# Performance work log

Measured on AMD Instinct MI355X. Metric: run time of the kernel, lower is better.

Reference implementation:

```python
import jax, jax.numpy as jnp
import numpy as np

N = 100000
E = 1600000
F = 64
THETA = (0.6, -0.4, 0.3, -0.2, 0.1)  # k = 5 polynomial coefficients


def setup_inputs() -> dict:
    key = jax.random.key(0)
    kx, ke = jax.random.split(key)
    x = jax.random.normal(kx, (N, F), dtype=jnp.float32)
    edge_index = jax.random.randint(ke, (2, E), 0, N, dtype=jnp.int64)
    return {"x": x, "edge_index": edge_index}


def _l_sym_mul(feat, src, dst, deg_inv_sqrt, n):
    # L_sym * feat = feat - D^{-1/2} A D^{-1/2} feat
    src_norm = feat[src] * deg_inv_sqrt[src]            # [E, F] gather + scale
    agg = jax.ops.segment_sum(src_norm, dst, num_segments=n)  # scatter-add to dst
    return feat - deg_inv_sqrt * agg


def reference(x, edge_index):
    src, dst = edge_index[0], edge_index[1]
    n = x.shape[0]
    # in-degree from dst, clamp to >= 1, D^{-1/2} as [N, 1]
    deg = jax.ops.segment_sum(jnp.ones((src.shape[0],), dtype=x.dtype), dst,
                              num_segments=n)
    deg = jnp.maximum(deg, 1.0)[:, None]
    deg_inv_sqrt = deg ** -0.5

    h_acc = THETA[0] * x
    feat = x
    for k in range(1, len(THETA)):
        feat = _l_sym_mul(feat, src, dst, deg_inv_sqrt, n)
        h_acc = h_acc + THETA[k] * feat
    return h_acc
```

## Files before the change

kernel.cpp:

```cpp
#include <hip/hip_runtime.h>
#include <hip/hip_fp16.h>


constexpr int kF = 64;
constexpr int BSHIFT = 8;
constexpr int NB = 1 << BSHIFT;
constexpr int TILE = 2048;
constexpr int KMAX = 512;

typedef unsigned nv4u __attribute__((ext_vector_type(4)));
typedef float    nv4f __attribute__((ext_vector_type(4)));

static __device__ __forceinline__ float hlo(unsigned u) {
    return __half2float(__ushort_as_half((unsigned short)(u & 0xffffu)));
}
static __device__ __forceinline__ float hhi(unsigned u) {
    return __half2float(__ushort_as_half((unsigned short)(u >> 16)));
}
static __device__ __forceinline__ unsigned pack2h(float a, float b) {
    return (unsigned)__half_as_ushort(__float2half_rn(a)) |
           ((unsigned)__half_as_ushort(__float2half_rn(b)) << 16);
}
static __device__ __forceinline__ unsigned padd2(unsigned a, unsigned b) {
    __half2 ha = *reinterpret_cast<__half2*>(&a);
    __half2 hb = *reinterpret_cast<__half2*>(&b);
    __half2 hc = __hadd2(ha, hb);
    return *reinterpret_cast<unsigned*>(&hc);
}

__global__ void k_binA(const int* __restrict__ src, const int* __restrict__ dst,
                       unsigned* __restrict__ pairs, int* __restrict__ gcursor,
                       const float4* __restrict__ x4, uint4* __restrict__ xb4,
                       int n8, int E, int K, int cap) {
    __shared__ int hist[KMAX];
    __shared__ int gb[KMAX];
    const int tid = threadIdx.x;
    const long long tb = (long long)blockIdx.x * TILE;
    const int tcount = (int)min((long long)TILE, (long long)E - tb);

    {
        int per = (n8 + gridDim.x - 1) / (int)gridDim.x;
        int b0 = blockIdx.x * per;
        int b1 = min(b0 + per, n8);
        for (int i = b0 + tid; i < b1; i += 512) {
            float4 a = x4[2 * i];
            float4 b = x4[2 * i + 1];
            uint4 o;
            o.x = pack2h(a.x, a.y);
            o.y = pack2h(a.z, a.w);
            o.z = pack2h(b.x, b.y);
            o.w = pack2h(b.z, b.w);
            xb4[i] = o;
        }
    }

    hist[tid] = 0;
    __syncthreads();
    int dc[4], sc[4];
    #pragma unroll
    for (int k = 0; k < 4; ++k) {
        int i = tid + k * 512;
        if (i < tcount) {
            dc[k] = dst[tb + i];
            sc[k] = src[tb + i];
            atomicAdd(&hist[dc[k] >> BSHIFT], 1);
        } else {
            dc[k] = -1;
        }
    }
    __syncthreads();
    int hv = hist[tid];
    gb[tid] = (tid < K && hv > 0) ? atomicAdd(&gcursor[tid], hv) : 0;
    hist[tid] = 0;
    __syncthreads();
    #pragma unroll
    for (int k = 0; k < 4; ++k) {
        if (dc[k] >= 0) {
            int d = dc[k];
            int b = d >> BSHIFT;
            int pos = atomicAdd(&hist[b], 1);
            pairs[(size_t)b * cap + gb[b] + pos] =
                ((unsigned)(d & (NB - 1)) << 23) | (unsigned)sc[k];
        }
    }
}

__global__ void k_binB(const unsigned* __restrict__ pairs, const int* __restrict__ gcursor,
                       int* __restrict__ rp, float* __restrict__ dinv2,
                       float* __restrict__ rdeg, int* __restrict__ csr,
                       const uint4* __restrict__ xb, uint4* __restrict__ g0,
                       int N, int E, int K, int cap) {
    __shared__ int gsc[KMAX];
    __shared__ int cnt[NB];
    __shared__ int stmp[NB];
    __shared__ int cur[NB];
    __shared__ float sdinv[NB];
    const int b = blockIdx.x;
    const int tid = threadIdx.x;

    if (b == 0 && tid < 8)
        g0[((size_t)N << 3) + tid] = make_uint4(0, 0, 0, 0);

    int gv = (tid < K) ? gcursor[tid] : 0;
    gsc[tid] = gv;
    __syncthreads();
    for (int o = 1; o < KMAX; o <<= 1) {
        int t = (tid >= o) ? gsc[tid - o] : 0;
        __syncthreads();
        gsc[tid] += t;
        __syncthreads();
    }
    const int ecnt = gcursor[b];
    const int base = gsc[b] - ecnt;
    const unsigned* bp = pairs + (size_t)b * cap;

    if (tid < NB) cnt[tid] = 0;
    __syncthreads();
    for (int i = tid; i < ecnt; i += 512)
        atomicAdd(&cnt[bp[i] >> 23], 1);
    __syncthreads();
    int v = (tid < NB) ? cnt[tid] : 0;
    if (tid < NB) stmp[tid] = v;
    __syncthreads();
    for (int o = 1; o < NB; o <<= 1) {
        int t = (tid >= o && tid < NB) ? stmp[tid - o] : 0;
        __syncthreads();
        if (tid < NB) stmp[tid] += t;
        __syncthreads();
    }
    int node = (b << BSHIFT) + tid;
    if (tid < NB) {
        int abs0 = base + stmp[tid] - v;
        cur[tid] = abs0;
        float d = fmaxf((float)v, 1.0f);
        sdinv[tid] = rsqrtf(d);
        if (node < N) {
            rp[node] = abs0;
            dinv2[node] = 1.0f / d;
            rdeg[node]  = sqrtf(d);
        }
    }
    if (b == K - 1 && tid == 0) rp[N] = E;
    __syncthreads();
    for (int i = tid; i < ecnt; i += 512) {
        unsigned p = bp[i];
        int pos = atomicAdd(&cur[p >> 23], 1);
        csr[pos] = (int)(p & 0x7FFFFFu);
    }
    const int nbase = b << BSHIFT;
    const int qmax = min(NB, N - nbase) << 3;
    const uint4* xbp = xb + ((size_t)nbase << 3);
    uint4* g0p = g0 + ((size_t)nbase << 3);
    for (int q = tid; q < qmax; q += 512) {
        float di = sdinv[q >> 3];
        uint4 xv = xbp[q];
        uint4 o;
        o.x = pack2h(di * hlo(xv.x), di * hhi(xv.x));
        o.y = pack2h(di * hlo(xv.y), di * hhi(xv.y));
        o.z = pack2h(di * hlo(xv.z), di * hhi(xv.z));
        o.w = pack2h(di * hlo(xv.w), di * hhi(xv.w));
        g0p[q] = o;
    }
}

template <bool LAST>
__global__ void k_gather(const int* __restrict__ rp, const int* __restrict__ csr,
                         const unsigned short* __restrict__ gin,
                         const float* __restrict__ dinv2,
                         unsigned short* __restrict__ gout,
                         const unsigned short* __restrict__ xb,
                         const unsigned short* __restrict__ g1t,
                         const unsigned short* __restrict__ g2t,
                         const float* __restrict__ rdeg,
                         float* __restrict__ h, int n,
                         float t0, float t1, float t2, float t3, float t4) {
    if (!LAST && blockIdx.x == 0 && threadIdx.x < 8)
        *(((uint4*)(gout + ((size_t)n << 6))) + threadIdx.x) = make_uint4(0, 0, 0, 0);

    int wid = (blockIdx.x * blockDim.x + threadIdx.x) >> 6;
    int lane = threadIdx.x & 63;
    int half = lane >> 5;
    int r = (lane >> 3) & 3;
    int c = lane & 7;
    int node = wid * 2 + half;
    if (wid * 2 >= n) return;
    bool valid = node < n;
    int beg = valid ? rp[node] : 0;
    int end = valid ? rp[node + 1] : 0;
    int len = end - beg;
    int olen = __shfl_xor(len, 32, 64);
    int mlen = (len > olen) ? len : olen;

    unsigned acc[4] = {0u, 0u, 0u, 0u};

    uint4 rc1 = make_uint4(0, 0, 0, 0), rc2 = make_uint4(0, 0, 0, 0);
    int sn1 = n, sn2 = n;
    if (mlen > 0) {
        int j1 = beg + r, j2 = j1 + 4;
        bool o1 = j1 < end, o2 = j2 < end;
        int s1 = csr[o1 ? j1 : 0]; s1 = o1 ? s1 : n;
        int s2 = csr[o2 ? j2 : 0]; s2 = o2 ? s2 : n;
        rc1 = *(const uint4*)(gin + ((size_t)s1 << 6) + (c << 3));
        rc2 = *(const uint4*)(gin + ((size_t)s2 << 6) + (c << 3));
        int j1b = beg + 8 + r, j2b = j1b + 4;
        bool vb = 8 < mlen;
        bool b1 = vb && (j1b < end), b2 = vb && (j2b < end);
        sn1 = csr[b1 ? j1b : 0]; sn1 = b1 ? sn1 : n;
        sn2 = csr[b2 ? j2b : 0]; sn2 = b2 ? sn2 : n;
    }
    for (int i = 0; i < mlen; i += 8) {
        uint4 rn1 = *(const uint4*)(gin + ((size_t)sn1 << 6) + (c << 3));
        uint4 rn2 = *(const uint4*)(gin + ((size_t)sn2 << 6) + (c << 3));
        int j1n = beg + i + 16 + r, j2n = j1n + 4;
        bool vn = (i + 16) < mlen;
        bool t1c = vn && (j1n < end), t2c = vn && (j2n < end);
        int st1 = csr[t1c ? j1n : 0]; st1 = t1c ? st1 : n;
        int st2 = csr[t2c ? j2n : 0]; st2 = t2c ? st2 : n;
        acc[0] = padd2(acc[0], rc1.x); acc[1] = padd2(acc[1], rc1.y);
        acc[2] = padd2(acc[2], rc1.z); acc[3] = padd2(acc[3], rc1.w);
        acc[0] = padd2(acc[0], rc2.x); acc[1] = padd2(acc[1], rc2.y);
        acc[2] = padd2(acc[2], rc2.z); acc[3] = padd2(acc[3], rc2.w);
        rc1 = rn1; rc2 = rn2;
        sn1 = st1; sn2 = st2;
    }
    #pragma unroll
    for (int m = 8; m <= 16; m <<= 1) {
        #pragma unroll
        for (int i = 0; i < 4; ++i)
            acc[i] = padd2(acc[i], __shfl_xor(acc[i], m, 64));
    }

    if (r == 0 && valid) {
        size_t off = ((size_t)node << 6) + (c << 3);
        uint4 rr = *(const uint4*)(gin + off);
        float d2 = dinv2[node];
        float v[8];
        v[0] = hlo(rr.x) - d2 * hlo(acc[0]); v[1] = hhi(rr.x) - d2 * hhi(acc[0]);
        v[2] = hlo(rr.y) - d2 * hlo(acc[1]); v[3] = hhi(rr.y) - d2 * hhi(acc[1]);
        v[4] = hlo(rr.z) - d2 * hlo(acc[2]); v[5] = hhi(rr.z) - d2 * hhi(acc[2]);
        v[6] = hlo(rr.w) - d2 * hlo(acc[3]); v[7] = hhi(rr.w) - d2 * hhi(acc[3]);
        if (!LAST) {
            nv4u o;
            o.x = pack2h(v[0], v[1]);
            o.y = pack2h(v[2], v[3]);
            o.z = pack2h(v[4], v[5]);
            o.w = pack2h(v[6], v[7]);
            __builtin_nontemporal_store(o, (nv4u*)(gout + off));
        } else {
            nv4u xv = __builtin_nontemporal_load((const nv4u*)(xb + off));
            nv4u a  = __builtin_nontemporal_load((const nv4u*)(g1t + off));
            nv4u b  = __builtin_nontemporal_load((const nv4u*)(g2t + off));
            float rd = rdeg[node];
            float s1 = rd * t1, s2 = rd * t2, s3 = rd * t3, s4 = rd * t4;
            nv4f h0, h1;
            h0.x = t0 * hlo(xv.x) + s1 * hlo(a.x) + s2 * hlo(b.x) + s3 * hlo(rr.x) + s4 * v[0];
            h0.y = t0 * hhi(xv.x) + s1 * hhi(a.x) + s2 * hhi(b.x) + s3 * hhi(rr.x) + s4 * v[1];
            h0.z = t0 * hlo(xv.y) + s1 * hlo(a.y) + s2 * hlo(b.y) + s3 * hlo(rr.y) + s4 * v[2];
            h0.w = t0 * hhi(xv.y) + s1 * hhi(a.y) + s2 * hhi(b.y) + s3 * hhi(rr.y) + s4 * v[3];
            h1.x = t0 * hlo(xv.z) + s1 * hlo(a.z) + s2 * hlo(b.z) + s3 * hlo(rr.z) + s4 * v[4];
            h1.y = t0 * hhi(xv.z) + s1 * hhi(a.z) + s2 * hhi(b.z) + s3 * hhi(rr.z) + s4 * v[5];
            h1.z = t0 * hlo(xv.w) + s1 * hlo(a.w) + s2 * hlo(b.w) + s3 * hlo(rr.w) + s4 * v[6];
            h1.w = t0 * hhi(xv.w) + s1 * hhi(a.w) + s2 * hhi(b.w) + s3 * hhi(rr.w) + s4 * v[7];
            __builtin_nontemporal_store(h0, (nv4f*)(h + off));
            __builtin_nontemporal_store(h1, (nv4f*)(h + off + 4));
        }
    }
}

extern "C" void kernel_launch(void* const* d_in, const int* in_sizes, int n_in,
                              void* d_out, int out_size, void* d_ws, size_t ws_size,
                              hipStream_t stream) {
    const float* x  = (const float*)d_in[0];
    const int*   ei = (const int*)d_in[1];
    const int N = in_sizes[0] / kF;
    const int E = in_sizes[1] / 2;
    const int* src = ei;
    const int* dst = ei + E;
    float* h = (float*)d_out;

    const int K = (N + NB - 1) >> BSHIFT;
    const int cap = 2 * ((E + K - 1) / K);

    char* ws = (char*)d_ws;
    size_t off = 0;
    auto carve = [&](size_t bytes) {
        void* p = ws + off;
        off = (off + bytes + 511) & ~(size_t)511;
        return p;
    };
    size_t gbytes = (size_t)(N + 1) * kF * 2;
    int*            gcursor = (int*)carve((size_t)K * 4);
    int*            rp      = (int*)carve((size_t)(N + 1) * 4);
    float*          dinv2   = (float*)carve((size_t)N * 4);
    float*          rdeg    = (float*)carve((size_t)N * 4);
    int*            csr     = (int*)carve((size_t)E * 4);
    unsigned short* xb      = (unsigned short*)carve((size_t)N * kF * 2);
    unsigned short* g0      = (unsigned short*)carve(gbytes);
    size_t pbytes = (size_t)K * cap * 4;
    unsigned short* g1      = (unsigned short*)carve(gbytes > pbytes ? gbytes : pbytes);
    unsigned short* g2      = (unsigned short*)carve(gbytes);
    unsigned short* g3      = (unsigned short*)carve(gbytes);
    unsigned*       pairs   = (unsigned*)g1;

    const float theta[5] = {0.6f, -0.4f, 0.3f, -0.2f, 0.1f};
    const int n8 = N * kF / 8;

    hipMemsetAsync(gcursor, 0, (size_t)K * 4, stream);
    k_binA<<<(E + TILE - 1) / TILE, 512, 0, stream>>>(src, dst, pairs, gcursor,
                                                      (const float4*)x, (uint4*)xb,
                                                      n8, E, K, cap);
    k_binB<<<K, 512, 0, stream>>>(pairs, gcursor, rp, dinv2, rdeg, csr,
                                  (const uint4*)xb, (uint4*)g0, N, E, K, cap);

    const int nwaves = (N + 1) / 2;
    const int gblocks = (nwaves + 3) / 4;
    k_gather<false><<<gblocks, 256, 0, stream>>>(rp, csr, g0, dinv2, g1,
                                                 nullptr, nullptr, nullptr, nullptr,
                                                 nullptr, N, 0, 0, 0, 0, 0);
    k_gather<false><<<gblocks, 256, 0, stream>>>(rp, csr, g1, dinv2, g2,
                                                 nullptr, nullptr, nullptr, nullptr,
                                                 nullptr, N, 0, 0, 0, 0, 0);
    k_gather<false><<<gblocks, 256, 0, stream>>>(rp, csr, g2, dinv2, g3,
                                                 nullptr, nullptr, nullptr, nullptr,
                                                 nullptr, N, 0, 0, 0, 0, 0);
    k_gather<true><<<gblocks, 256, 0, stream>>>(rp, csr, g3, dinv2, nullptr,
                                                xb, g1, g2, rdeg, h, N,
                                                theta[0], theta[1], theta[2],
                                                theta[3], theta[4]);
}
```

Baseline: 244.5 us.

## Split feature matrix into four 16-column planes and gather per plane

Stores the fp16 feature arrays as four separate planes of 16 features per node, and launches each SpMM gather pass over all four planes. Each lane reads 16 bytes of a 32-byte row slice, so a wave now covers 16 neighbours per load instead of 4. The aim is that each plane (about 3.2 MB) fits better in cache during the random gathers. In exchange, CSR indices and row pointers are re-read four times per pass, the grid is four times larger, and the shuffle reduction gets longer. CSR loads are also switched to nontemporal.

New measurement: 497.1 us. 103% more time.

```diff
diff --git a/kernel.cpp b/kernel.cpp
--- a/kernel.cpp
+++ b/kernel.cpp
@@ -3,6 +3,8 @@
 
 
 constexpr int kF = 64;
+constexpr int CH = 4;
+constexpr int CF = 16;
 constexpr int BSHIFT = 8;
 constexpr int NB = 1 << BSHIFT;
 constexpr int TILE = 2048;
@@ -27,16 +29,20 @@
     __half2 hc = __hadd2(ha, hb);
     return *reinterpret_cast<unsigned*>(&hc);
 }
+static __device__ __forceinline__ int ntl_i(const int* p) {
+    return __builtin_nontemporal_load(p);
+}
 
 __global__ void k_binA(const int* __restrict__ src, const int* __restrict__ dst,
                        unsigned* __restrict__ pairs, int* __restrict__ gcursor,
                        const float4* __restrict__ x4, uint4* __restrict__ xb4,
-                       int n8, int E, int K, int cap) {
+                       int n8, int N, int E, int K, int cap) {
     __shared__ int hist[KMAX];
     __shared__ int gb[KMAX];
     const int tid = threadIdx.x;
     const long long tb = (long long)blockIdx.x * TILE;
     const int tcount = (int)min((long long)TILE, (long long)E - tb);
+    const size_t ps4 = (size_t)(N + 1) * 2;
 
     {
         int per = (n8 + gridDim.x - 1) / (int)gridDim.x;
@@ -50,7 +56,9 @@
             o.y = pack2h(a.z, a.w);
             o.z = pack2h(b.x, b.y);
             o.w = pack2h(b.z, b.w);
-            xb4[i] = o;
+            int nloc = i >> 3, sub = i & 7;
+            int c = sub >> 1, dd = sub & 1;
+            xb4[(size_t)c * ps4 + (size_t)nloc * 2 + dd] = o;
         }
     }
 
@@ -88,7 +96,7 @@
 __global__ void k_binB(const unsigned* __restrict__ pairs, const int* __restrict__ gcursor,
                        int* __restrict__ rp, float* __restrict__ dinv2,
                        float* __restrict__ rdeg, int* __restrict__ csr,
-                       const uint4* __restrict__ xb, uint4* __restrict__ g0,
+                       const uint4* __restrict__ xb4, uint4* __restrict__ g04,
                        int N, int E, int K, int cap) {
     __shared__ int gsc[KMAX];
     __shared__ int cnt[NB];
@@ -97,9 +105,10 @@
     __shared__ float sdinv[NB];
     const int b = blockIdx.x;
     const int tid = threadIdx.x;
+    const size_t ps4 = (size_t)(N + 1) * 2;
 
     if (b == 0 && tid < 8)
-        g0[((size_t)N << 3) + tid] = make_uint4(0, 0, 0, 0);
+        g04[(size_t)(tid >> 1) * ps4 + (size_t)N * 2 + (tid & 1)] = make_uint4(0, 0, 0, 0);
 
     int gv = (tid < K) ? gcursor[tid] : 0;
     gsc[tid] = gv;
@@ -148,18 +157,20 @@
         csr[pos] = (int)(p & 0x7FFFFFu);
     }
     const int nbase = b << BSHIFT;
-    const int qmax = min(NB, N - nbase) << 3;
-    const uint4* xbp = xb + ((size_t)nbase << 3);
-    uint4* g0p = g0 + ((size_t)nbase << 3);
-    for (int q = tid; q < qmax; q += 512) {
-        float di = sdinv[q >> 3];
-        uint4 xv = xbp[q];
-        uint4 o;
-        o.x = pack2h(di * hlo(xv.x), di * hhi(xv.x));
-        o.y = pack2h(di * hlo(xv.y), di * hhi(xv.y));
-        o.z = pack2h(di * hlo(xv.z), di * hhi(xv.z));
-        o.w = pack2h(di * hlo(xv.w), di * hhi(xv.w));
-        g0p[q] = o;
+    const int nn = min(NB, N - nbase);
+    for (int c = 0; c < CH; ++c) {
+        const uint4* xp = xb4 + (size_t)c * ps4 + (size_t)nbase * 2;
+        uint4*       gp = g04 + (size_t)c * ps4 + (size_t)nbase * 2;
+        for (int q = tid; q < nn * 2; q += 512) {
+            float di = sdinv[q >> 1];
+            uint4 xv = xp[q];
+            uint4 o;
+            o.x = pack2h(di * hlo(xv.x), di * hhi(xv.x));
+            o.y = pack2h(di * hlo(xv.y), di * hhi(xv.y));
+            o.z = pack2h(di * hlo(xv.z), di * hhi(xv.z));
+            o.w = pack2h(di * hlo(xv.w), di * hhi(xv.w));
+            gp[q] = o;
+        }
     }
 }
 
@@ -172,17 +183,22 @@
                          const unsigned short* __restrict__ g1t,
                          const unsigned short* __restrict__ g2t,
                          const float* __restrict__ rdeg,
-                         float* __restrict__ h, int n,
+                         float* __restrict__ h, int n, int cblocks,
                          float t0, float t1, float t2, float t3, float t4) {
-    if (!LAST && blockIdx.x == 0 && threadIdx.x < 8)
-        *(((uint4*)(gout + ((size_t)n << 6))) + threadIdx.x) = make_uint4(0, 0, 0, 0);
-
-    int wid = (blockIdx.x * blockDim.x + threadIdx.x) >> 6;
-    int lane = threadIdx.x & 63;
-    int half = lane >> 5;
-    int r = (lane >> 3) & 3;
-    int c = lane & 7;
-    int node = wid * 2 + half;
+    const size_t ps = (size_t)(n + 1) * CF;
+    if (!LAST && blockIdx.x == 0 && threadIdx.x < 8) {
+        int p = threadIdx.x >> 1, cc = threadIdx.x & 1;
+        *(uint4*)(gout + (size_t)p * ps + (size_t)n * CF + cc * 8) = make_uint4(0, 0, 0, 0);
+    }
+
+    const int chunk = blockIdx.x / cblocks;
+    const int bidx  = blockIdx.x - chunk * cblocks;
+    const int wid   = bidx * 4 + (threadIdx.x >> 6);
+    const int lane  = threadIdx.x & 63;
+    const int half  = lane >> 5;
+    const int r     = (lane >> 1) & 15;
+    const int c     = lane & 1;
+    const int node  = wid * 2 + half;
     if (wid * 2 >= n) return;
     bool valid = node < n;
     int beg = valid ? rp[node] : 0;
@@ -191,31 +207,33 @@
     int olen = __shfl_xor(len, 32, 64);
     int mlen = (len > olen) ? len : olen;
 
+    const unsigned short* gp = gin + (size_t)chunk * ps;
+
     unsigned acc[4] = {0u, 0u, 0u, 0u};
 
     uint4 rc1 = make_uint4(0, 0, 0, 0), rc2 = make_uint4(0, 0, 0, 0);
     int sn1 = n, sn2 = n;
     if (mlen > 0) {
-        int j1 = beg + r, j2 = j1 + 4;
+        int j1 = beg + r, j2 = j1 + 16;
         bool o1 = j1 < end, o2 = j2 < end;
-        int s1 = csr[o1 ? j1 : 0]; s1 = o1 ? s1 : n;
-        int s2 = csr[o2 ? j2 : 0]; s2 = o2 ? s2 : n;
-        rc1 = *(const uint4*)(gin + ((size_t)s1 << 6) + (c << 3));
-        rc2 = *(const uint4*)(gin + ((size_t)s2 << 6) + (c << 3));
-        int j1b = beg + 8 + r, j2b = j1b + 4;
-        bool vb = 8 < mlen;
+        int s1 = ntl_i(csr + (o1 ? j1 : 0)); s1 = o1 ? s1 : n;
+        int s2 = ntl_i(csr + (o2 ? j2 : 0)); s2 = o2 ? s2 : n;
+        rc1 = *(const uint4*)(gp + ((size_t)s1 << 4) + (c << 3));
+        rc2 = *(const uint4*)(gp + ((size_t)s2 << 4) + (c << 3));
+        int j1b = beg + 32 + r, j2b = j1b + 16;
+        bool vb = 32 < mlen;
         bool b1 = vb && (j1b < end), b2 = vb && (j2b < end);
-        sn1 = csr[b1 ? j1b : 0]; sn1 = b1 ? sn1 : n;
-        sn2 = csr[b2 ? j2b : 0]; sn2 = b2 ? sn2 : n;
-    }
-    for (int i = 0; i < mlen; i += 8) {
-        uint4 rn1 = *(const uint4*)(gin + ((size_t)sn1 << 6) + (c << 3));
-        uint4 rn2 = *(const uint4*)(gin + ((size_t)sn2 << 6) + (c << 3));
-        int j1n = beg + i + 16 + r, j2n = j1n + 4;
-        bool vn = (i + 16) < mlen;
+        sn1 = ntl_i(csr + (b1 ? j1b : 0)); sn1 = b1 ? sn1 : n;
+        sn2 = ntl_i(csr + (b2 ? j2b : 0)); sn2 = b2 ? sn2 : n;
+    }
+    for (int i = 0; i < mlen; i += 32) {
+        uint4 rn1 = *(const uint4*)(gp + ((size_t)sn1 << 4) + (c << 3));
+        uint4 rn2 = *(const uint4*)(gp + ((size_t)sn2 << 4) + (c << 3));
+        int j1n = beg + i + 64 + r, j2n = j1n + 16;
+        bool vn = (i + 64) < mlen;
         bool t1c = vn && (j1n < end), t2c = vn && (j2n < end);
-        int st1 = csr[t1c ? j1n : 0]; st1 = t1c ? st1 : n;
-        int st2 = csr[t2c ? j2n : 0]; st2 = t2c ? st2 : n;
+        int st1 = ntl_i(csr + (t1c ? j1n : 0)); st1 = t1c ? st1 : n;
+        int st2 = ntl_i(csr + (t2c ? j2n : 0)); st2 = t2c ? st2 : n;
         acc[0] = padd2(acc[0], rc1.x); acc[1] = padd2(acc[1], rc1.y);
         acc[2] = padd2(acc[2], rc1.z); acc[3] = padd2(acc[3], rc1.w);
         acc[0] = padd2(acc[0], rc2.x); acc[1] = padd2(acc[1], rc2.y);
@@ -224,14 +242,14 @@
         sn1 = st1; sn2 = st2;
     }
     #pragma unroll
-    for (int m = 8; m <= 16; m <<= 1) {
+    for (int m = 2; m <= 16; m <<= 1) {
         #pragma unroll
         for (int i = 0; i < 4; ++i)
             acc[i] = padd2(acc[i], __shfl_xor(acc[i], m, 64));
     }
 
     if (r == 0 && valid) {
-        size_t off = ((size_t)node << 6) + (c << 3);
+        size_t off = (size_t)chunk * ps + ((size_t)node << 4) + (c << 3);
         uint4 rr = *(const uint4*)(gin + off);
         float d2 = dinv2[node];
         float v[8];
@@ -261,8 +279,9 @@
             h1.y = t0 * hhi(xv.z) + s1 * hhi(a.z) + s2 * hhi(b.z) + s3 * hhi(rr.z) + s4 * v[5];
             h1.z = t0 * hlo(xv.w) + s1 * hlo(a.w) + s2 * hlo(b.w) + s3 * hlo(rr.w) + s4 * v[6];
             h1.w = t0 * hhi(xv.w) + s1 * hhi(a.w) + s2 * hhi(b.w) + s3 * hhi(rr.w) + s4 * v[7];
-            __builtin_nontemporal_store(h0, (nv4f*)(h + off));
-            __builtin_nontemporal_store(h1, (nv4f*)(h + off + 4));
+            size_t hoff = (size_t)node * kF + chunk * CF + (c << 3);
+            __builtin_nontemporal_store(h0, (nv4f*)(h + hoff));
+            __builtin_nontemporal_store(h1, (nv4f*)(h + hoff + 4));
         }
     }
 }
@@ -288,13 +307,13 @@
         off = (off + bytes + 511) & ~(size_t)511;
         return p;
     };
-    size_t gbytes = (size_t)(N + 1) * kF * 2;
+    size_t gbytes = (size_t)CH * (N + 1) * CF * 2;
     int*            gcursor = (int*)carve((size_t)K * 4);
     int*            rp      = (int*)carve((size_t)(N + 1) * 4);
     float*          dinv2   = (float*)carve((size_t)N * 4);
     float*          rdeg    = (float*)carve((size_t)N * 4);
     int*            csr     = (int*)carve((size_t)E * 4);
-    unsigned short* xb      = (unsigned short*)carve((size_t)N * kF * 2);
+    unsigned short* xb      = (unsigned short*)carve(gbytes);
     unsigned short* g0      = (unsigned short*)carve(gbytes);
     size_t pbytes = (size_t)K * cap * 4;
     unsigned short* g1      = (unsigned short*)carve(gbytes > pbytes ? gbytes : pbytes);
@@ -308,23 +327,24 @@
     hipMemsetAsync(gcursor, 0, (size_t)K * 4, stream);
     k_binA<<<(E + TILE - 1) / TILE, 512, 0, stream>>>(src, dst, pairs, gcursor,
                                                       (const float4*)x, (uint4*)xb,
-                                                      n8, E, K, cap);
+                                                      n8, N, E, K, cap);
     k_binB<<<K, 512, 0, stream>>>(pairs, gcursor, rp, dinv2, rdeg, csr,
                                   (const uint4*)xb, (uint4*)g0, N, E, K, cap);
 
     const int nwaves = (N + 1) / 2;
-    const int gblocks = (nwaves + 3) / 4;
+    const int cblocks = (nwaves + 3) / 4;
+    const int gblocks = CH * cblocks;
     k_gather<false><<<gblocks, 256, 0, stream>>>(rp, csr, g0, dinv2, g1,
                                                  nullptr, nullptr, nullptr, nullptr,
-                                                 nullptr, N, 0, 0, 0, 0, 0);
+                                                 nullptr, N, cblocks, 0, 0, 0, 0, 0);
     k_gather<false><<<gblocks, 256, 0, stream>>>(rp, csr, g1, dinv2, g2,
                                                  nullptr, nullptr, nullptr, nullptr,
-                                                 nullptr, N, 0, 0, 0, 0, 0);
+                                                 nullptr, N, cblocks, 0, 0, 0, 0, 0);
     k_gather<false><<<gblocks, 256, 0, stream>>>(rp, csr, g2, dinv2, g3,
                                                  nullptr, nullptr, nullptr, nullptr,
-                                                 nullptr, N, 0, 0, 0, 0, 0);
+                                                 nullptr, N, cblocks, 0, 0, 0, 0, 0);
     k_gather<true><<<gblocks, 256, 0, stream>>>(rp, csr, g3, dinv2, nullptr,
-                                                xb, g1, g2, rdeg, h, N,
+                                                xb, g1, g2, rdeg, h, N, cblocks,
                                                 theta[0], theta[1], theta[2],
                                                 theta[3], theta[4]);
 }
```

## Replace two-pass bucket binning CSR build with global degree histogram and atomic scatter

Applied to the files above, without the earlier changes.

CSR construction switches from bucketed pair binning, with a per-bucket local sort in shared memory, to three passes. A global per-node degree atomic histogram, a scan kernel that builds row pointers and cursors, and a scatter kernel that uses global atomics on per-node cursors to place source indices. This removes the intermediate pairs buffer and its write and read-back. In exchange it adds global atomics per edge (two passes over dst), a larger memset, and an extra kernel launch. The scatter also loses locality, so the neighbour order within each row becomes nondeterministic.

New measurement: 429.0 us. 75.4% more time.

```diff
diff --git a/kernel.cpp b/kernel.cpp
--- a/kernel.cpp
+++ b/kernel.cpp
@@ -28,12 +28,11 @@
     return *reinterpret_cast<unsigned*>(&hc);
 }
 
-__global__ void k_binA(const int* __restrict__ src, const int* __restrict__ dst,
-                       unsigned* __restrict__ pairs, int* __restrict__ gcursor,
+__global__ void k_hist(const int* __restrict__ dst, int* __restrict__ deg,
+                       int* __restrict__ btot,
                        const float4* __restrict__ x4, uint4* __restrict__ xb4,
-                       int n8, int E, int K, int cap) {
+                       int n8, int E) {
     __shared__ int hist[KMAX];
-    __shared__ int gb[KMAX];
     const int tid = threadIdx.x;
     const long long tb = (long long)blockIdx.x * TILE;
     const int tcount = (int)min((long long)TILE, (long long)E - tb);
@@ -56,44 +55,27 @@
 
     hist[tid] = 0;
     __syncthreads();
-    int dc[4], sc[4];
     #pragma unroll
     for (int k = 0; k < 4; ++k) {
         int i = tid + k * 512;
         if (i < tcount) {
-            dc[k] = dst[tb + i];
-            sc[k] = src[tb + i];
-            atomicAdd(&hist[dc[k] >> BSHIFT], 1);
-        } else {
-            dc[k] = -1;
+            int d = __builtin_nontemporal_load(dst + tb + i);
+            atomicAdd(&deg[d], 1);
+            atomicAdd(&hist[d >> BSHIFT], 1);
         }
     }
     __syncthreads();
     int hv = hist[tid];
-    gb[tid] = (tid < K && hv > 0) ? atomicAdd(&gcursor[tid], hv) : 0;
-    hist[tid] = 0;
-    __syncthreads();
-    #pragma unroll
-    for (int k = 0; k < 4; ++k) {
-        if (dc[k] >= 0) {
-            int d = dc[k];
-            int b = d >> BSHIFT;
-            int pos = atomicAdd(&hist[b], 1);
-            pairs[(size_t)b * cap + gb[b] + pos] =
-                ((unsigned)(d & (NB - 1)) << 23) | (unsigned)sc[k];
-        }
-    }
-}
-
-__global__ void k_binB(const unsigned* __restrict__ pairs, const int* __restrict__ gcursor,
-                       int* __restrict__ rp, float* __restrict__ dinv2,
-                       float* __restrict__ rdeg, int* __restrict__ csr,
+    if (hv > 0) atomicAdd(&btot[tid], hv);
+}
+
+__global__ void k_scan(const int* __restrict__ btot, const int* __restrict__ deg,
+                       int* __restrict__ rp, int* __restrict__ cur,
+                       float* __restrict__ dinv2, float* __restrict__ rdeg,
                        const uint4* __restrict__ xb, uint4* __restrict__ g0,
-                       int N, int E, int K, int cap) {
+                       int N, int E, int K) {
     __shared__ int gsc[KMAX];
-    __shared__ int cnt[NB];
     __shared__ int stmp[NB];
-    __shared__ int cur[NB];
     __shared__ float sdinv[NB];
     const int b = blockIdx.x;
     const int tid = threadIdx.x;
@@ -101,8 +83,7 @@
     if (b == 0 && tid < 8)
         g0[((size_t)N << 3) + tid] = make_uint4(0, 0, 0, 0);
 
-    int gv = (tid < K) ? gcursor[tid] : 0;
-    gsc[tid] = gv;
+    gsc[tid] = (tid < K) ? btot[tid] : 0;
     __syncthreads();
     for (int o = 1; o < KMAX; o <<= 1) {
         int t = (tid >= o) ? gsc[tid - o] : 0;
@@ -110,16 +91,10 @@
         gsc[tid] += t;
         __syncthreads();
     }
-    const int ecnt = gcursor[b];
-    const int base = gsc[b] - ecnt;
-    const unsigned* bp = pairs + (size_t)b * cap;
-
-    if (tid < NB) cnt[tid] = 0;
-    __syncthreads();
-    for (int i = tid; i < ecnt; i += 512)
-        atomicAdd(&cnt[bp[i] >> 23], 1);
-    __syncthreads();
-    int v = (tid < NB) ? cnt[tid] : 0;
+    const int base = gsc[b] - btot[b];
+
+    int node = (b << BSHIFT) + tid;
+    int v = (tid < NB && node < N) ? deg[node] : 0;
     if (tid < NB) stmp[tid] = v;
     __syncthreads();
     for (int o = 1; o < NB; o <<= 1) {
@@ -128,25 +103,19 @@
         if (tid < NB) stmp[tid] += t;
         __syncthreads();
     }
-    int node = (b << BSHIFT) + tid;
     if (tid < NB) {
         int abs0 = base + stmp[tid] - v;
-        cur[tid] = abs0;
         float d = fmaxf((float)v, 1.0f);
         sdinv[tid] = rsqrtf(d);
         if (node < N) {
-            rp[node] = abs0;
+            rp[node]  = abs0;
+            cur[node] = abs0;
             dinv2[node] = 1.0f / d;
             rdeg[node]  = sqrtf(d);
         }
     }
     if (b == K - 1 && tid == 0) rp[N] = E;
     __syncthreads();
-    for (int i = tid; i < ecnt; i += 512) {
-        unsigned p = bp[i];
-        int pos = atomicAdd(&cur[p >> 23], 1);
-        csr[pos] = (int)(p & 0x7FFFFFu);
-    }
     const int nbase = b << BSHIFT;
     const int qmax = min(NB, N - nbase) << 3;
     const uint4* xbp = xb + ((size_t)nbase << 3);
@@ -160,6 +129,23 @@
         o.z = pack2h(di * hlo(xv.z), di * hhi(xv.z));
         o.w = pack2h(di * hlo(xv.w), di * hhi(xv.w));
         g0p[q] = o;
+    }
+}
+
+__global__ void k_scatter(const int* __restrict__ src, const int* __restrict__ dst,
+                          int* __restrict__ cur, int* __restrict__ csr, int E) {
+    const int tid = threadIdx.x;
+    const long long tb = (long long)blockIdx.x * TILE;
+    const int tcount = (int)min((long long)TILE, (long long)E - tb);
+    #pragma unroll
+    for (int k = 0; k < 4; ++k) {
+        int i = tid + k * 512;
+        if (i < tcount) {
+            int d = __builtin_nontemporal_load(dst + tb + i);
+            int s = __builtin_nontemporal_load(src + tb + i);
+            int pos = atomicAdd(&cur[d], 1);
+            __builtin_nontemporal_store(s, csr + pos);
+        }
     }
 }
 
@@ -279,7 +265,6 @@
     float* h = (float*)d_out;
 
     const int K = (N + NB - 1) >> BSHIFT;
-    const int cap = 2 * ((E + K - 1) / K);
 
     char* ws = (char*)d_ws;
     size_t off = 0;
@@ -289,28 +274,29 @@
         return p;
     };
     size_t gbytes = (size_t)(N + 1) * kF * 2;
-    int*            gcursor = (int*)carve((size_t)K * 4);
+    int*            btot    = (int*)carve((size_t)(KMAX + N) * 4);
+    int*            deg     = btot + KMAX;
     int*            rp      = (int*)carve((size_t)(N + 1) * 4);
+    int*            cur     = (int*)carve((size_t)N * 4);
     float*          dinv2   = (float*)carve((size_t)N * 4);
     float*          rdeg    = (float*)carve((size_t)N * 4);
     int*            csr     = (int*)carve((size_t)E * 4);
     unsigned short* xb      = (unsigned short*)carve((size_t)N * kF * 2);
     unsigned short* g0      = (unsigned short*)carve(gbytes);
-    size_t pbytes = (size_t)K * cap * 4;
-    unsigned short* g1      = (unsigned short*)carve(gbytes > pbytes ? gbytes : pbytes);
+    unsigned short* g1      = (unsigned short*)carve(gbytes);
     unsigned short* g2      = (unsigned short*)carve(gbytes);
     unsigned short* g3      = (unsigned short*)carve(gbytes);
-    unsigned*       pairs   = (unsigned*)g1;
 
     const float theta[5] = {0.6f, -0.4f, 0.3f, -0.2f, 0.1f};
     const int n8 = N * kF / 8;
-
-    hipMemsetAsync(gcursor, 0, (size_t)K * 4, stream);
-    k_binA<<<(E + TILE - 1) / TILE, 512, 0, stream>>>(src, dst, pairs, gcursor,
-                                                      (const float4*)x, (uint4*)xb,
-                                                      n8, E, K, cap);
-    k_binB<<<K, 512, 0, stream>>>(pairs, gcursor, rp, dinv2, rdeg, csr,
-                                  (const uint4*)xb, (uint4*)g0, N, E, K, cap);
+    const int eblocks = (E + TILE - 1) / TILE;
+
+    hipMemsetAsync(btot, 0, (size_t)(KMAX + N) * 4, stream);
+    k_hist<<<eblocks, 512, 0, stream>>>(dst, deg, btot,
+                                        (const float4*)x, (uint4*)xb, n8, E);
+    k_scan<<<K, 512, 0, stream>>>(btot, deg, rp, cur, dinv2, rdeg,
+                                  (const uint4*)xb, (uint4*)g0, N, E, K);
+    k_scatter<<<eblocks, 512, 0, stream>>>(src, dst, cur, csr, E);
 
     const int nwaves = (N + 1) / 2;
     const int gblocks = (nwaves + 3) / 4;
```

## Sort nodes by in-degree so gather waves process similar-length rows

Applied to the files above, without the earlier changes.

Adds a degree histogram, a scan and a counting-sort pass that build a permutation of nodes ordered by in-degree. The four gather passes then map each half-wave to a node through this permutation, so the two nodes sharing a wave have similar neighbour counts and less lane divergence. This costs three extra small kernel launches and an extra indirection per node. Output writes and reads of the node's own row are no longer contiguous across waves, which loses some locality.

Result: slower. 265.2 us (+8.5%).

```diff
diff --git a/kernel.cpp b/kernel.cpp
--- a/kernel.cpp
+++ b/kernel.cpp
@@ -7,6 +7,7 @@
 constexpr int NB = 1 << BSHIFT;
 constexpr int TILE = 2048;
 constexpr int KMAX = 512;
+constexpr int DBINS = 512;
 
 typedef unsigned nv4u __attribute__((ext_vector_type(4)));
 typedef float    nv4f __attribute__((ext_vector_type(4)));
@@ -87,7 +88,8 @@
 
 __global__ void k_binB(const unsigned* __restrict__ pairs, const int* __restrict__ gcursor,
                        int* __restrict__ rp, float* __restrict__ dinv2,
-                       float* __restrict__ rdeg, int* __restrict__ csr,
+                       float* __restrict__ rdeg, int* __restrict__ degw,
+                       int* __restrict__ csr,
                        const uint4* __restrict__ xb, uint4* __restrict__ g0,
                        int N, int E, int K, int cap) {
     __shared__ int gsc[KMAX];
@@ -138,6 +140,7 @@
             rp[node] = abs0;
             dinv2[node] = 1.0f / d;
             rdeg[node]  = sqrtf(d);
+            degw[node]  = v;
         }
     }
     if (b == K - 1 && tid == 0) rp[N] = E;
@@ -163,8 +166,56 @@
     }
 }
 
+__global__ void k_dhist(const int* __restrict__ deg, int* __restrict__ dbin, int N) {
+    __shared__ int h[DBINS];
+    int tid = threadIdx.x;
+    h[tid] = 0;
+    __syncthreads();
+    int i = blockIdx.x * DBINS + tid;
+    if (i < N) atomicAdd(&h[min(deg[i], DBINS - 1)], 1);
+    __syncthreads();
+    if (h[tid] > 0) atomicAdd(&dbin[tid], h[tid]);
+}
+
+__global__ void k_dscan(const int* __restrict__ dbin, int* __restrict__ dcur) {
+    __shared__ int s[DBINS];
+    int tid = threadIdx.x;
+    int own = dbin[tid];
+    s[tid] = own;
+    __syncthreads();
+    for (int o = 1; o < DBINS; o <<= 1) {
+        int t = (tid >= o) ? s[tid - o] : 0;
+        __syncthreads();
+        s[tid] += t;
+        __syncthreads();
+    }
+    dcur[tid] = s[tid] - own;
+}
+
+__global__ void k_dperm(const int* __restrict__ deg, int* __restrict__ dcur,
+                        int* __restrict__ perm, int N) {
+    __shared__ int h[DBINS];
+    __shared__ int gb[DBINS];
+    int tid = threadIdx.x;
+    h[tid] = 0;
+    __syncthreads();
+    int i = blockIdx.x * DBINS + tid;
+    int d = (i < N) ? min(deg[i], DBINS - 1) : -1;
+    if (d >= 0) atomicAdd(&h[d], 1);
+    __syncthreads();
+    int hv = h[tid];
+    gb[tid] = (hv > 0) ? atomicAdd(&dcur[tid], hv) : 0;
+    h[tid] = 0;
+    __syncthreads();
+    if (d >= 0) {
+        int pos = atomicAdd(&h[d], 1);
+        perm[gb[d] + pos] = i;
+    }
+}
+
 template <bool LAST>
 __global__ void k_gather(const int* __restrict__ rp, const int* __restrict__ csr,
+                         const int* __restrict__ perm,
                          const unsigned short* __restrict__ gin,
                          const float* __restrict__ dinv2,
                          unsigned short* __restrict__ gout,
@@ -182,9 +233,10 @@
     int half = lane >> 5;
     int r = (lane >> 3) & 3;
     int c = lane & 7;
-    int node = wid * 2 + half;
+    int idx = wid * 2 + half;
     if (wid * 2 >= n) return;
-    bool valid = node < n;
+    bool valid = idx < n;
+    int node = valid ? perm[idx] : 0;
     int beg = valid ? rp[node] : 0;
     int end = valid ? rp[node + 1] : 0;
     int len = end - beg;
@@ -289,7 +341,11 @@
         return p;
     };
     size_t gbytes = (size_t)(N + 1) * kF * 2;
-    int*            gcursor = (int*)carve((size_t)K * 4);
+    int*            gcursor = (int*)carve((size_t)KMAX * 4);
+    int*            dbin    = (int*)carve((size_t)DBINS * 4);
+    int*            dcur    = (int*)carve((size_t)DBINS * 4);
+    int*            deg     = (int*)carve((size_t)N * 4);
+    int*            perm    = (int*)carve((size_t)N * 4);
     int*            rp      = (int*)carve((size_t)(N + 1) * 4);
     float*          dinv2   = (float*)carve((size_t)N * 4);
     float*          rdeg    = (float*)carve((size_t)N * 4);
@@ -304,26 +360,31 @@
 
     const float theta[5] = {0.6f, -0.4f, 0.3f, -0.2f, 0.1f};
     const int n8 = N * kF / 8;
-
-    hipMemsetAsync(gcursor, 0, (size_t)K * 4, stream);
+    const int dblocks = (N + DBINS - 1) / DBINS;
+
+    hipMemsetAsync(gcursor, 0, (size_t)(KMAX + DBINS) * 4, stream);
     k_binA<<<(E + TILE - 1) / TILE, 512, 0, stream>>>(src, dst, pairs, gcursor,
                                                       (const float4*)x, (uint4*)xb,
                                                       n8, E, K, cap);
-    k_binB<<<K, 512, 0, stream>>>(pairs, gcursor, rp, dinv2, rdeg, csr,
+    k_binB<<<K, 512, 0, stream>>>(pairs, gcursor, rp, dinv2, rdeg, deg, csr,
                                   (const uint4*)xb, (uint4*)g0, N, E, K, cap);
+
+    k_dhist<<<dblocks, DBINS, 0, stream>>>(deg, dbin, N);
+    k_dscan<<<1, DBINS, 0, stream>>>(dbin, dcur);
+    k_dperm<<<dblocks, DBINS, 0, stream>>>(deg, dcur, perm, N);
 
     const int nwaves = (N + 1) / 2;
     const int gblocks = (nwaves + 3) / 4;
-    k_gather<false><<<gblocks, 256, 0, stream>>>(rp, csr, g0, dinv2, g1,
+    k_gather<false><<<gblocks, 256, 0, stream>>>(rp, csr, perm, g0, dinv2, g1,
                                                  nullptr, nullptr, nullptr, nullptr,
                                                  nullptr, N, 0, 0, 0, 0, 0);
-    k_gather<false><<<gblocks, 256, 0, stream>>>(rp, csr, g1, dinv2, g2,
+    k_gather<false><<<gblocks, 256, 0, stream>>>(rp, csr, perm, g1, dinv2, g2,
                                                  nullptr, nullptr, nullptr, nullptr,
                                                  nullptr, N, 0, 0, 0, 0, 0);
-    k_gather<false><<<gblocks, 256, 0, stream>>>(rp, csr, g2, dinv2, g3,
+    k_gather<false><<<gblocks, 256, 0, stream>>>(rp, csr, perm, g2, dinv2, g3,
                                                  nullptr, nullptr, nullptr, nullptr,
                                                  nullptr, N, 0, 0, 0, 0, 0);
-    k_gather<true><<<gblocks, 256, 0, stream>>>(rp, csr, g3, dinv2, nullptr,
+    k_gather<true><<<gblocks, 256, 0, stream>>>(rp, csr, perm, g3, dinv2, nullptr,
                                                 xb, g1, g2, rdeg, h, N,
                                                 theta[0], theta[1], theta[2],
                                                 theta[3], theta[4]);
```
